# Optimization experiments

Hardware: AMD Instinct MI355X
Metric: run time of the kernel (lower is better)

## Reference

```python
import jax, jax.numpy as jnp
import numpy as np

N_ENT = 100000
N_REL = 24
N_BASES = 8
HID = 256
N_EDGES = 1000000
N_TRIPLES = 65536


def _rgcn_layer(x, src, dst, edge_type, norm, basis, comp, root, bias):
    # x: [N, d]; basis: [B, d, d]; comp: [R, B]; root: [d, d]; bias: [d]
    x_src = x[src]                    # [E, d] gather
    coef = comp[edge_type]            # [E, B]
    out = x @ root + bias             # root/self transform
    # W_r = sum_b comp[r,b] * basis_b is linear, so aggregate coefficient- and
    # norm-weighted source features per basis, then apply basis once at node level.
    for b in range(basis.shape[0]):
        w = (coef[:, b] * norm)[:, None] * x_src          # [E, d]
        agg = jax.ops.segment_sum(w, dst, num_segments=N_ENT)  # [N, d]
        out = out + agg @ basis[b]
    return out


def _edge_norm(dst, edge_type):
    # PyG RGCNConv propagates per relation with aggr='mean': normalize by
    # in-degree of dst counted within each relation type.
    key = dst * N_REL + edge_type
    cnt = jax.ops.segment_sum(jnp.ones_like(key, dtype=jnp.float32), key,
                              num_segments=N_ENT * N_REL)
    return 1.0 / jnp.maximum(cnt[key], 1.0)


def setup_inputs() -> dict:
    key = jax.random.key(0)
    ks = jax.random.split(key, 16)
    d = HID
    xav_e = float(np.sqrt(6.0 / (N_ENT + d)))
    xav_r = float(np.sqrt(6.0 / (N_REL + d)))
    xav_w = float(np.sqrt(6.0 / (d + d)))
    inp = {
        'entity_emb': jax.random.uniform(ks[0], (N_ENT, d), jnp.float32, -xav_e, xav_e),
        'rel_emb': jax.random.uniform(ks[1], (N_REL, d), jnp.float32, -xav_r, xav_r),
        'basis1': jax.random.uniform(ks[2], (N_BASES, d, d), jnp.float32, -xav_w, xav_w),
        'comp1': jax.random.normal(ks[3], (N_REL, N_BASES), jnp.float32) / np.sqrt(N_BASES),
        'root1': jax.random.uniform(ks[4], (d, d), jnp.float32, -xav_w, xav_w),
        'bias1': jnp.zeros((d,), jnp.float32),
        'basis2': jax.random.uniform(ks[5], (N_BASES, d, d), jnp.float32, -xav_w, xav_w),
        'comp2': jax.random.normal(ks[6], (N_REL, N_BASES), jnp.float32) / np.sqrt(N_BASES),
        'root2': jax.random.uniform(ks[7], (d, d), jnp.float32, -xav_w, xav_w),
        'bias2': jnp.zeros((d,), jnp.float32),
        'edge_index': jax.random.randint(ks[8], (2, N_EDGES), 0, N_ENT, jnp.int32),
        'edge_type': jax.random.randint(ks[9], (N_EDGES,), 0, N_REL, jnp.int32),
        'heads': jax.random.randint(ks[10], (N_TRIPLES,), 0, N_ENT, jnp.int32),
        'rels': jax.random.randint(ks[11], (N_TRIPLES,), 0, N_REL, jnp.int32),
        'tails': jax.random.randint(ks[12], (N_TRIPLES,), 0, N_ENT, jnp.int32),
    }
    return inp


def reference(entity_emb, rel_emb, basis1, comp1, root1, bias1,
              basis2, comp2, root2, bias2,
              edge_index, edge_type, heads, rels, tails):
    src, dst = edge_index[0], edge_index[1]
    norm = _edge_norm(dst, edge_type)
    # eval mode: no edge dropout, feature dropout is identity
    x = entity_emb
    x = jax.nn.relu(_rgcn_layer(x, src, dst, edge_type, norm, basis1, comp1, root1, bias1))
    x = jax.nn.relu(_rgcn_layer(x, src, dst, edge_type, norm, basis2, comp2, root2, bias2))
    # DistMult score: sum(h * r * t)
    scores = jnp.sum(x[heads] * rel_emb[rels] * x[tails], axis=-1)
    return scores
```

## Files before the change

### kernel.cpp

```cpp
#include <hip/hip_runtime.h>
#include <hip/hip_bf16.h>

#define N_ENT   100000
#define N_REL   24
#define N_BASES 8
#define HID     256
#define N_EDGES 1000000
#define N_TRIPLES 65536


typedef __attribute__((ext_vector_type(8))) short bf16x8;
typedef __attribute__((ext_vector_type(4))) float f32x4;

__device__ __forceinline__ void atomF(float* p, float v) {
#if defined(__HIP_PLATFORM_AMD__)
    unsafeAtomicAdd(p, v);
#else
    atomicAdd(p, v);
#endif
}

__device__ __forceinline__ unsigned short f2bf(float f) {
    unsigned int u = __builtin_bit_cast(unsigned int, f);
    u += 0x7fffu + ((u >> 16) & 1u);
    return (unsigned short)(u >> 16);
}
__device__ __forceinline__ float bf2f(unsigned short h) {
    return __builtin_bit_cast(float, (unsigned int)h << 16);
}

__global__ __launch_bounds__(256) void count_kernel(
    const int* __restrict__ src, const int* __restrict__ dst,
    const int* __restrict__ et, int* __restrict__ cnt, int* __restrict__ hist)
{
    __shared__ int lhist[N_REL];
    if (threadIdx.x < N_REL) lhist[threadIdx.x] = 0;
    __syncthreads();
    int stride = gridDim.x * blockDim.x;
    for (int e = blockIdx.x * blockDim.x + threadIdx.x; e < N_EDGES; e += stride) {
        int d = dst[e], t = et[e];
        atomicAdd(&cnt[d * N_REL + t], 1);
        atomicAdd(&lhist[t], 1);
    }
    __syncthreads();
    if (threadIdx.x < N_REL) atomicAdd(&hist[threadIdx.x], lhist[threadIdx.x]);
}

__global__ void prefix_kernel(const int* __restrict__ hist, int* offs,
                              int* cursor, int* tileoffs)
{
    if (threadIdx.x == 0) {
        int off = 0, toff = 0;
        for (int r = 0; r < N_REL; ++r) {
            offs[r] = off; cursor[r] = off; tileoffs[r] = toff;
            off  += hist[r];
            toff += (hist[r] + 63) >> 6;
        }
        offs[N_REL] = off; tileoffs[N_REL] = toff;
    }
}

#define SC_CHUNK 512
__global__ __launch_bounds__(256) void scatter_kernel(
    const int* __restrict__ src, const int* __restrict__ dst,
    const int* __restrict__ et, const int* __restrict__ cnt, int* cursor,
    int* __restrict__ srcS, int* __restrict__ dstS, float* __restrict__ normS)
{
    __shared__ int lhist[N_REL];
    __shared__ int lbase[N_REL];
    int tid = threadIdx.x;
    int base_e = blockIdx.x * SC_CHUNK;
    if (tid < N_REL) lhist[tid] = 0;
    __syncthreads();
    int myrank[2], myet[2];
    #pragma unroll
    for (int q = 0; q < 2; ++q) {
        int e = base_e + q * 256 + tid;
        if (e < N_EDGES) { myet[q] = et[e]; myrank[q] = atomicAdd(&lhist[myet[q]], 1); }
    }
    __syncthreads();
    if (tid < N_REL && lhist[tid] > 0) lbase[tid] = atomicAdd(&cursor[tid], lhist[tid]);
    __syncthreads();
    #pragma unroll
    for (int q = 0; q < 2; ++q) {
        int e = base_e + q * 256 + tid;
        if (e < N_EDGES) {
            int pos = lbase[myet[q]] + myrank[q];
            int d = dst[e];
            srcS[pos] = src[e];
            dstS[pos] = d;
            normS[pos] = 1.0f / (float)max(cnt[d * N_REL + myet[q]], 1);
        }
    }
}

__global__ __launch_bounds__(256) void makew_pk(
    const float* __restrict__ basis, const float* __restrict__ comp,
    unsigned short* __restrict__ Wh, unsigned short* __restrict__ Wl)
{
    int idx = blockIdx.x * 256 + threadIdx.x;
    if (idx >= N_REL * 8 * 4 * 256) return;
    int col = idx & 255;
    int q   = (idx >> 8) & 3;
    int kb  = (idx >> 10) & 7;
    int r   = idx >> 13;
    float cf[N_BASES];
    #pragma unroll
    for (int b = 0; b < N_BASES; ++b) cf[b] = comp[r * N_BASES + b];
    unsigned short hh[8] __attribute__((aligned(16)));
    unsigned short ll[8] __attribute__((aligned(16)));
    #pragma unroll
    for (int j = 0; j < 8; ++j) {
        int k = kb * 32 + q * 8 + j;
        float acc = 0.f;
        #pragma unroll
        for (int b = 0; b < N_BASES; ++b)
            acc += cf[b] * basis[(b << 16) + (k << 8) + col];
        unsigned short h = f2bf(acc);
        unsigned short l = f2bf(acc - bf2f(h));
        hh[j] = h; ll[j] = l;
    }
    size_t base = ((size_t)(r * 8 + kb) * 256 + col) * 32 + q * 8;
    *(uint4*)&Wh[base] = *(const uint4*)hh;
    *(uint4*)&Wl[base] = *(const uint4*)ll;
}

template <bool RELU_IN>
__global__ __launch_bounds__(256) void root_gemm(
    const float* __restrict__ x, const float* __restrict__ root,
    const float* __restrict__ bias, float* __restrict__ out)
{
    __shared__ float As[64][HID];
    int tid = threadIdx.x;
    int row0 = blockIdx.x * 64;
    for (int it = 0; it < 16; ++it) {
        int row = (it << 2) + (tid >> 6);
        int c4  = (tid & 63) << 2;
        int grow = row0 + row;
        float4 v = make_float4(0.f, 0.f, 0.f, 0.f);
        if (grow < N_ENT) v = *(const float4*)(x + (size_t)grow * HID + c4);
        if (RELU_IN) {
            v.x = fmaxf(v.x, 0.f); v.y = fmaxf(v.y, 0.f);
            v.z = fmaxf(v.z, 0.f); v.w = fmaxf(v.w, 0.f);
        }
        *(float4*)&As[row][c4] = v;
    }
    __syncthreads();
    int eg = tid >> 5, cg = tid & 31;
    const float* wp = root + (cg << 3);
    float acc[8][8] = {{0.f}};
    for (int k = 0; k < HID; k += 4) {
        float4 a4[8];
        #pragma unroll
        for (int i = 0; i < 8; ++i) a4[i] = *(const float4*)&As[(eg << 3) + i][k];
        #pragma unroll
        for (int kk = 0; kk < 4; ++kk) {
            float4 w0 = *(const float4*)(wp + (size_t)(k + kk) * HID);
            float4 w1 = *(const float4*)(wp + (size_t)(k + kk) * HID + 4);
            #pragma unroll
            for (int i = 0; i < 8; ++i) {
                float a = kk == 0 ? a4[i].x : kk == 1 ? a4[i].y : kk == 2 ? a4[i].z : a4[i].w;
                acc[i][0] += a * w0.x; acc[i][1] += a * w0.y;
                acc[i][2] += a * w0.z; acc[i][3] += a * w0.w;
                acc[i][4] += a * w1.x; acc[i][5] += a * w1.y;
                acc[i][6] += a * w1.z; acc[i][7] += a * w1.w;
            }
        }
    }
    float4 b0 = *(const float4*)(bias + (cg << 3));
    float4 b1 = *(const float4*)(bias + (cg << 3) + 4);
    #pragma unroll
    for (int i = 0; i < 8; ++i) {
        int grow = row0 + (eg << 3) + i;
        if (grow < N_ENT) {
            float4 o0 = make_float4(acc[i][0] + b0.x, acc[i][1] + b0.y,
                                    acc[i][2] + b0.z, acc[i][3] + b0.w);
            float4 o1 = make_float4(acc[i][4] + b1.x, acc[i][5] + b1.y,
                                    acc[i][6] + b1.z, acc[i][7] + b1.w);
            *(float4*)(out + (size_t)grow * HID + (cg << 3))     = o0;
            *(float4*)(out + (size_t)grow * HID + (cg << 3) + 4) = o1;
        }
    }
}

template <bool RELU_IN>
__global__ __launch_bounds__(256, 4) void edge_gemm_mfma(
    const float* __restrict__ x,
    const unsigned short* __restrict__ Wh, const unsigned short* __restrict__ Wl,
    const int* __restrict__ srcS, const int* __restrict__ dstS,
    const float* __restrict__ normS, const int* __restrict__ offs,
    const int* __restrict__ tileoffs, float* __restrict__ out)
{
    __shared__ unsigned short Ah[64 * 128];
    __shared__ unsigned short Al[64 * 128];
    int b = blockIdx.x;
    if (b >= tileoffs[N_REL]) return;
    int r = 0;
    while (tileoffs[r + 1] <= b) ++r;
    int e0 = offs[r] + ((b - tileoffs[r]) << 6);
    int e1 = min(offs[r + 1], e0 + 64);
    int ne = e1 - e0;

    int tid = threadIdx.x;
    int wv = tid >> 6;
    int lane = tid & 63;
    int lc = lane & 15, lq = lane >> 4;
    const unsigned short* WhR = Wh + ((size_t)r << 16);
    const unsigned short* WlR = Wl + ((size_t)r << 16);

    f32x4 acc[4][4];
    #pragma unroll
    for (int mi = 0; mi < 4; ++mi)
        #pragma unroll
        for (int ni = 0; ni < 4; ++ni) acc[mi][ni] = (f32x4)0.f;

    for (int h = 0; h < 2; ++h) {
        for (int it = 0; it < 8; ++it) {
            int row = (it << 3) + (tid >> 5);
            int cc  = (tid & 31) << 2;
            float4 v = make_float4(0.f, 0.f, 0.f, 0.f);
            float nrm = 0.f;
            if (row < ne) {
                int s = srcS[e0 + row];
                nrm = normS[e0 + row];
                v = *(const float4*)(x + (size_t)s * HID + (h << 7) + cc);
            }
            if (RELU_IN) {
                v.x = fmaxf(v.x, 0.f); v.y = fmaxf(v.y, 0.f);
                v.z = fmaxf(v.z, 0.f); v.w = fmaxf(v.w, 0.f);
            }
            v.x *= nrm; v.y *= nrm; v.z *= nrm; v.w *= nrm;
            unsigned short hh[4] __attribute__((aligned(8)));
            unsigned short ll[4] __attribute__((aligned(8)));
            float vv[4] = {v.x, v.y, v.z, v.w};
            #pragma unroll
            for (int j = 0; j < 4; ++j) {
                unsigned short hb = f2bf(vv[j]);
                hh[j] = hb;
                ll[j] = f2bf(vv[j] - bf2f(hb));
            }
            int byt = (cc << 1) ^ ((row & 7) << 4);
            int us  = (row << 7) + (byt >> 1);
            *(ushort4*)&Ah[us] = *(const ushort4*)hh;
            *(ushort4*)&Al[us] = *(const ushort4*)ll;
        }
        __syncthreads();

        for (int kb = 0; kb < 4; ++kb) {
            int kbf = (h << 2) + kb;
            bf16x8 ah[4], al[4], bh[4], bl[4];
            #pragma unroll
            for (int mi = 0; mi < 4; ++mi) {
                int row = mi * 16 + lc;
                int byt = ((kb << 6) + (lq << 4)) ^ ((row & 7) << 4);
                int us  = (row << 7) + (byt >> 1);
                ah[mi] = *(const bf16x8*)&Ah[us];
                al[mi] = *(const bf16x8*)&Al[us];
            }
            #pragma unroll
            for (int ni = 0; ni < 4; ++ni) {
                int col = (wv << 6) + ni * 16 + lc;
                size_t bidx = ((size_t)(kbf << 8) + col) * 32 + (lq << 3);
                bh[ni] = *(const bf16x8*)&WhR[bidx];
                bl[ni] = *(const bf16x8*)&WlR[bidx];
            }
            #pragma unroll
            for (int mi = 0; mi < 4; ++mi)
                #pragma unroll
                for (int ni = 0; ni < 4; ++ni) {
                    acc[mi][ni] = __builtin_amdgcn_mfma_f32_16x16x32_bf16(
                        ah[mi], bh[ni], acc[mi][ni], 0, 0, 0);
                    acc[mi][ni] = __builtin_amdgcn_mfma_f32_16x16x32_bf16(
                        ah[mi], bl[ni], acc[mi][ni], 0, 0, 0);
                    acc[mi][ni] = __builtin_amdgcn_mfma_f32_16x16x32_bf16(
                        al[mi], bh[ni], acc[mi][ni], 0, 0, 0);
                }
        }
        if (h == 0) __syncthreads();
    }

    #pragma unroll
    for (int mi = 0; mi < 4; ++mi) {
        #pragma unroll
        for (int rr = 0; rr < 4; ++rr) {
            int e = mi * 16 + (lq << 2) + rr;
            if (e < ne) {
                int drow = dstS[e0 + e];
                float* op = out + (size_t)drow * HID + (wv << 6) + lc;
                #pragma unroll
                for (int ni = 0; ni < 4; ++ni)
                    atomF(op + ni * 16, acc[mi][ni][rr]);
            }
        }
    }
}

__global__ __launch_bounds__(256) void distmult_kernel(
    const float* __restrict__ h2, const float* __restrict__ rel,
    const int* __restrict__ heads, const int* __restrict__ rels,
    const int* __restrict__ tails, float* __restrict__ scores)
{
    int tid = threadIdx.x;
    int tr = blockIdx.x * 4 + (tid >> 6);
    int lane = tid & 63;
    if (tr >= N_TRIPLES) return;
    int h = heads[tr], r = rels[tr], t = tails[tr];
    float4 a = *(const float4*)(h2 + (size_t)h * HID + lane * 4);
    float4 bb = *(const float4*)(rel + (size_t)r * HID + lane * 4);
    float4 c = *(const float4*)(h2 + (size_t)t * HID + lane * 4);
    a.x = fmaxf(a.x, 0.f); a.y = fmaxf(a.y, 0.f); a.z = fmaxf(a.z, 0.f); a.w = fmaxf(a.w, 0.f);
    c.x = fmaxf(c.x, 0.f); c.y = fmaxf(c.y, 0.f); c.z = fmaxf(c.z, 0.f); c.w = fmaxf(c.w, 0.f);
    float acc = a.x * bb.x * c.x + a.y * bb.y * c.y + a.z * bb.z * c.z + a.w * bb.w * c.w;
    #pragma unroll
    for (int off = 32; off >= 1; off >>= 1) acc += __shfl_xor(acc, off, 64);
    if (lane == 0) scores[tr] = acc;
}

extern "C" void kernel_launch(void* const* d_in, const int* in_sizes, int n_in,
                              void* d_out, int out_size, void* d_ws, size_t ws_size,
                              hipStream_t stream)
{
    const float* entity  = (const float*)d_in[0];
    const float* rel_emb = (const float*)d_in[1];
    const float* basis1  = (const float*)d_in[2];
    const float* comp1   = (const float*)d_in[3];
    const float* root1   = (const float*)d_in[4];
    const float* bias1   = (const float*)d_in[5];
    const float* basis2  = (const float*)d_in[6];
    const float* comp2   = (const float*)d_in[7];
    const float* root2   = (const float*)d_in[8];
    const float* bias2   = (const float*)d_in[9];
    const int* eidx  = (const int*)d_in[10];
    const int* etype = (const int*)d_in[11];
    const int* heads = (const int*)d_in[12];
    const int* rels  = (const int*)d_in[13];
    const int* tails = (const int*)d_in[14];
    const int* src = eidx;
    const int* dst = eidx + N_EDGES;

    char* ws = (char*)d_ws;
    int*   cnt      = (int*)(ws + 0);
    int*   small    = (int*)(ws + 9600000);
    int*   hist     = small;
    int*   offs     = small + 32;
    int*   cursor   = small + 64;
    int*   tileoffs = small + 96;
    int*   srcS  = (int*)(ws + 9604096);
    int*   dstS  = (int*)(ws + 13604096);
    float* normS = (float*)(ws + 17604096);
    unsigned short* Whi = (unsigned short*)(ws + 21604096);
    unsigned short* Wlo = (unsigned short*)(ws + 24749824);
    float* h1    = (float*)(ws + 27895552);
    float* h2    = (float*)(ws + 130295552);

    hipMemsetAsync(cnt, 0, (size_t)N_ENT * N_REL * sizeof(int), stream);
    hipMemsetAsync(small, 0, 4096, stream);

    count_kernel<<<2048, 256, 0, stream>>>(src, dst, etype, cnt, hist);
    prefix_kernel<<<1, 64, 0, stream>>>(hist, offs, cursor, tileoffs);
    scatter_kernel<<<(N_EDGES + SC_CHUNK - 1) / SC_CHUNK, 256, 0, stream>>>(
        src, dst, etype, cnt, cursor, srcS, dstS, normS);

    int egrid = N_EDGES / 64 + N_REL;
    int rgrid = (N_ENT + 63) / 64;
    int wgrid = (N_REL * 8 * 4 * 256 + 255) / 256;

    makew_pk<<<wgrid, 256, 0, stream>>>(basis1, comp1, Whi, Wlo);
    root_gemm<false><<<rgrid, 256, 0, stream>>>(entity, root1, bias1, h1);
    edge_gemm_mfma<false><<<egrid, 256, 0, stream>>>(
        entity, Whi, Wlo, srcS, dstS, normS, offs, tileoffs, h1);

    makew_pk<<<wgrid, 256, 0, stream>>>(basis2, comp2, Whi, Wlo);
    root_gemm<true><<<rgrid, 256, 0, stream>>>(h1, root2, bias2, h2);
    edge_gemm_mfma<true><<<egrid, 256, 0, stream>>>(
        h1, Whi, Wlo, srcS, dstS, normS, offs, tileoffs, h2);

    distmult_kernel<<<N_TRIPLES / 4, 256, 0, stream>>>(
        h2, rel_emb, heads, rels, tails, (float*)d_out);
}
```

Baseline: 2.996 ms.

## Replace atomic scatter-add with two-phase edge buffer and CSR segment reduction

The edge GEMM writes each per-edge message into a temporary buffer, ordered by destination, using non-temporal stores instead of float atomics into the output. A per-destination degree count, prefix scan and rank kernel build CSR offsets, and a segmented reduction kernel sums the messages into the node features. This removes contended global atomics but adds about 1 GB of write-then-read traffic plus several extra kernels. It only runs when the workspace is large enough, otherwise the atomic path is used.

```diff
diff --git a/kernel.cpp b/kernel.cpp
--- a/kernel.cpp
+++ b/kernel.cpp
@@ -8,6 +8,22 @@
 #define N_EDGES 1000000
 #define N_TRIPLES 65536
 
+#define OFF_CNT    0ull
+#define OFF_DEG    9600000ull
+#define OFF_SMALL  10000000ull
+#define OFF_SRCS   10004096ull
+#define OFF_DSTS   14004096ull
+#define OFF_NORMS  18004096ull
+#define OFF_WHI    22004096ull
+#define OFF_WLO    25149824ull
+#define OFF_H1     28295552ull
+#define OFF_H2     130695552ull
+#define OFF_DRANK  233095552ull
+#define OFF_ROWPTR 237095552ull
+#define OFF_CUR2   237495680ull
+#define OFF_BSUM   237895680ull
+#define OFF_TMP    237897728ull
+#define NEED_TOTAL 1261897728ull
 
 typedef __attribute__((ext_vector_type(8))) short bf16x8;
 typedef __attribute__((ext_vector_type(4))) float f32x4;
@@ -19,7 +35,9 @@
     atomicAdd(p, v);
 #endif
 }
-
+__device__ __forceinline__ void ntstore(float* p, float v) {
+    __builtin_nontemporal_store(v, p);
+}
 __device__ __forceinline__ unsigned short f2bf(float f) {
     unsigned int u = __builtin_bit_cast(unsigned int, f);
     u += 0x7fffu + ((u >> 16) & 1u);
@@ -31,7 +49,8 @@
 
 __global__ __launch_bounds__(256) void count_kernel(
     const int* __restrict__ src, const int* __restrict__ dst,
-    const int* __restrict__ et, int* __restrict__ cnt, int* __restrict__ hist)
+    const int* __restrict__ et, int* __restrict__ cnt, int* __restrict__ hist,
+    int* __restrict__ deg)
 {
     __shared__ int lhist[N_REL];
     if (threadIdx.x < N_REL) lhist[threadIdx.x] = 0;
@@ -40,6 +59,7 @@
     for (int e = blockIdx.x * blockDim.x + threadIdx.x; e < N_EDGES; e += stride) {
         int d = dst[e], t = et[e];
         atomicAdd(&cnt[d * N_REL + t], 1);
+        atomicAdd(&deg[d], 1);
         atomicAdd(&lhist[t], 1);
     }
     __syncthreads();
@@ -92,6 +112,62 @@
             normS[pos] = 1.0f / (float)max(cnt[d * N_REL + myet[q]], 1);
         }
     }
+}
+
+#define SCAN_NB 391
+__global__ __launch_bounds__(256) void scan_k1(
+    const int* __restrict__ deg, int* __restrict__ rowptr, int* __restrict__ bsum)
+{
+    __shared__ int s[256];
+    int i = threadIdx.x, b = blockIdx.x;
+    int g = b * 256 + i;
+    int v = (g < N_ENT) ? deg[g] : 0;
+    s[i] = v;
+    __syncthreads();
+    for (int off = 1; off < 256; off <<= 1) {
+        int t = (i >= off) ? s[i - off] : 0;
+        __syncthreads();
+        s[i] += t;
+        __syncthreads();
+    }
+    if (g < N_ENT) rowptr[g] = s[i] - v;
+    if (i == 255) bsum[b] = s[255];
+}
+
+__global__ __launch_bounds__(512) void scan_k2(int* __restrict__ bsum,
+                                               int* __restrict__ rowptr)
+{
+    __shared__ int s[512];
+    int i = threadIdx.x;
+    int v = (i < SCAN_NB) ? bsum[i] : 0;
+    s[i] = v;
+    __syncthreads();
+    for (int off = 1; off < 512; off <<= 1) {
+        int t = (i >= off) ? s[i - off] : 0;
+        __syncthreads();
+        s[i] += t;
+        __syncthreads();
+    }
+    if (i < SCAN_NB) bsum[i] = s[i] - v;
+    if (i == SCAN_NB - 1) rowptr[N_ENT] = s[i];
+}
+
+__global__ __launch_bounds__(256) void scan_k3(
+    int* __restrict__ rowptr, const int* __restrict__ bsum, int* __restrict__ cur2)
+{
+    int g = blockIdx.x * 256 + threadIdx.x;
+    if (g < N_ENT) {
+        int v = rowptr[g] + bsum[blockIdx.x];
+        rowptr[g] = v;
+        cur2[g] = v;
+    }
+}
+
+__global__ __launch_bounds__(256) void drank_kernel(
+    const int* __restrict__ dstS, int* __restrict__ cur2, int* __restrict__ drank)
+{
+    int p = blockIdx.x * 256 + threadIdx.x;
+    if (p < N_EDGES) drank[p] = atomicAdd(&cur2[dstS[p]], 1);
 }
 
 __global__ __launch_bounds__(256) void makew_pk(
@@ -183,13 +259,14 @@
     }
 }
 
-template <bool RELU_IN>
+template <bool RELU_IN, int MODE>
 __global__ __launch_bounds__(256, 4) void edge_gemm_mfma(
     const float* __restrict__ x,
     const unsigned short* __restrict__ Wh, const unsigned short* __restrict__ Wl,
     const int* __restrict__ srcS, const int* __restrict__ dstS,
     const float* __restrict__ normS, const int* __restrict__ offs,
-    const int* __restrict__ tileoffs, float* __restrict__ out)
+    const int* __restrict__ tileoffs, float* __restrict__ outp,
+    const int* __restrict__ drank)
 {
     __shared__ unsigned short Ah[64 * 128];
     __shared__ unsigned short Al[64 * 128];
@@ -285,14 +362,49 @@
         for (int rr = 0; rr < 4; ++rr) {
             int e = mi * 16 + (lq << 2) + rr;
             if (e < ne) {
-                int drow = dstS[e0 + e];
-                float* op = out + (size_t)drow * HID + (wv << 6) + lc;
-                #pragma unroll
-                for (int ni = 0; ni < 4; ++ni)
-                    atomF(op + ni * 16, acc[mi][ni][rr]);
-            }
-        }
-    }
+                if (MODE == 0) {
+                    int drow = dstS[e0 + e];
+                    float* op = outp + (size_t)drow * HID + (wv << 6) + lc;
+                    #pragma unroll
+                    for (int ni = 0; ni < 4; ++ni)
+                        atomF(op + ni * 16, acc[mi][ni][rr]);
+                } else {
+                    int pos = drank[e0 + e];
+                    float* op = outp + ((size_t)pos << 8) + (wv << 6) + lc;
+                    #pragma unroll
+                    for (int ni = 0; ni < 4; ++ni)
+                        ntstore(op + ni * 16, acc[mi][ni][rr]);
+                }
+            }
+        }
+    }
+}
+
+__global__ __launch_bounds__(256) void seg_reduce(
+    const float* __restrict__ tmp, const int* __restrict__ rowptr,
+    float* __restrict__ out)
+{
+    int d = blockIdx.x * 4 + (threadIdx.x >> 6);
+    if (d >= N_ENT) return;
+    int lane = threadIdx.x & 63;
+    int j0 = rowptr[d], j1 = rowptr[d + 1];
+    f32x4 acc = (f32x4)0.f;
+    int j = j0;
+    for (; j + 1 < j1; j += 2) {
+        f32x4 v0 = __builtin_nontemporal_load(
+            (const f32x4*)(tmp + ((size_t)j << 8) + (lane << 2)));
+        f32x4 v1 = __builtin_nontemporal_load(
+            (const f32x4*)(tmp + ((size_t)(j + 1) << 8) + (lane << 2)));
+        acc += v0 + v1;
+    }
+    if (j < j1) {
+        acc += __builtin_nontemporal_load(
+            (const f32x4*)(tmp + ((size_t)j << 8) + (lane << 2)));
+    }
+    float* op = out + (size_t)d * HID + (lane << 2);
+    f32x4 o = *(const f32x4*)op;
+    o += acc;
+    *(f32x4*)op = o;
 }
 
 __global__ __launch_bounds__(256) void distmult_kernel(
@@ -339,41 +451,68 @@
     const int* dst = eidx + N_EDGES;
 
     char* ws = (char*)d_ws;
-    int*   cnt      = (int*)(ws + 0);
-    int*   small    = (int*)(ws + 9600000);
+    int*   cnt      = (int*)(ws + OFF_CNT);
+    int*   deg      = (int*)(ws + OFF_DEG);
+    int*   small    = (int*)(ws + OFF_SMALL);
     int*   hist     = small;
     int*   offs     = small + 32;
     int*   cursor   = small + 64;
     int*   tileoffs = small + 96;
-    int*   srcS  = (int*)(ws + 9604096);
-    int*   dstS  = (int*)(ws + 13604096);
-    float* normS = (float*)(ws + 17604096);
-    unsigned short* Whi = (unsigned short*)(ws + 21604096);
-    unsigned short* Wlo = (unsigned short*)(ws + 24749824);
-    float* h1    = (float*)(ws + 27895552);
-    float* h2    = (float*)(ws + 130295552);
-
-    hipMemsetAsync(cnt, 0, (size_t)N_ENT * N_REL * sizeof(int), stream);
-    hipMemsetAsync(small, 0, 4096, stream);
-
-    count_kernel<<<2048, 256, 0, stream>>>(src, dst, etype, cnt, hist);
+    int*   srcS   = (int*)(ws + OFF_SRCS);
+    int*   dstS   = (int*)(ws + OFF_DSTS);
+    float* normS  = (float*)(ws + OFF_NORMS);
+    unsigned short* Whi = (unsigned short*)(ws + OFF_WHI);
+    unsigned short* Wlo = (unsigned short*)(ws + OFF_WLO);
+    float* h1     = (float*)(ws + OFF_H1);
+    float* h2     = (float*)(ws + OFF_H2);
+    int*   drank  = (int*)(ws + OFF_DRANK);
+    int*   rowptr = (int*)(ws + OFF_ROWPTR);
+    int*   cur2   = (int*)(ws + OFF_CUR2);
+    int*   bsum   = (int*)(ws + OFF_BSUM);
+    float* tmp    = (float*)(ws + OFF_TMP);
+
+    const bool two_phase = (ws_size >= NEED_TOTAL);
+
+    hipMemsetAsync(ws, 0, OFF_SMALL + 4096, stream);
+
+    count_kernel<<<2048, 256, 0, stream>>>(src, dst, etype, cnt, hist, deg);
     prefix_kernel<<<1, 64, 0, stream>>>(hist, offs, cursor, tileoffs);
     scatter_kernel<<<(N_EDGES + SC_CHUNK - 1) / SC_CHUNK, 256, 0, stream>>>(
         src, dst, etype, cnt, cursor, srcS, dstS, normS);
 
+    if (two_phase) {
+        scan_k1<<<SCAN_NB, 256, 0, stream>>>(deg, rowptr, bsum);
+        scan_k2<<<1, 512, 0, stream>>>(bsum, rowptr);
+        scan_k3<<<SCAN_NB, 256, 0, stream>>>(rowptr, bsum, cur2);
+        drank_kernel<<<(N_EDGES + 255) / 256, 256, 0, stream>>>(dstS, cur2, drank);
+    }
+
     int egrid = N_EDGES / 64 + N_REL;
     int rgrid = (N_ENT + 63) / 64;
     int wgrid = (N_REL * 8 * 4 * 256 + 255) / 256;
+    int sgrid = (N_ENT + 3) / 4;
 
     makew_pk<<<wgrid, 256, 0, stream>>>(basis1, comp1, Whi, Wlo);
     root_gemm<false><<<rgrid, 256, 0, stream>>>(entity, root1, bias1, h1);
-    edge_gemm_mfma<false><<<egrid, 256, 0, stream>>>(
-        entity, Whi, Wlo, srcS, dstS, normS, offs, tileoffs, h1);
+    if (two_phase) {
+        edge_gemm_mfma<false, 1><<<egrid, 256, 0, stream>>>(
+            entity, Whi, Wlo, srcS, dstS, normS, offs, tileoffs, tmp, drank);
+        seg_reduce<<<sgrid, 256, 0, stream>>>(tmp, rowptr, h1);
+    } else {
+        edge_gemm_mfma<false, 0><<<egrid, 256, 0, stream>>>(
+            entity, Whi, Wlo, srcS, dstS, normS, offs, tileoffs, h1, drank);
+    }
 
     makew_pk<<<wgrid, 256, 0, stream>>>(basis2, comp2, Whi, Wlo);
     root_gemm<true><<<rgrid, 256, 0, stream>>>(h1, root2, bias2, h2);
-    edge_gemm_mfma<true><<<egrid, 256, 0, stream>>>(
-        h1, Whi, Wlo, srcS, dstS, normS, offs, tileoffs, h2);
+    if (two_phase) {
+        edge_gemm_mfma<true, 1><<<egrid, 256, 0, stream>>>(
+            h1, Whi, Wlo, srcS, dstS, normS, offs, tileoffs, tmp, drank);
+        seg_reduce<<<sgrid, 256, 0, stream>>>(tmp, rowptr, h2);
+    } else {
+        edge_gemm_mfma<true, 0><<<egrid, 256, 0, stream>>>(
+            h1, Whi, Wlo, srcS, dstS, normS, offs, tileoffs, h2, drank);
+    }
 
     distmult_kernel<<<N_TRIPLES / 4, 256, 0, stream>>>(
         h2, rel_emb, heads, rels, tails, (float*)d_out);
```

Result: no change. 2.974 ms (-0.7%).
